# Performance work log

Measured on AMD Instinct MI355X. Metric: run time of the kernel, lower is better.

The kernel has to match this reference:

```python
import jax, jax.numpy as jnp
import numpy as np

B, S, D = 2, 2048, 1024
H, KV, HD = 16, 4, 64
E, TOPK, F = 8, 2, 2048
EPS = 1e-5
THETA = 10000.0


def setup_inputs() -> dict:
    key = jax.random.key(0)
    ks = jax.random.split(key, 12)
    sc = 0.02
    x = jax.random.normal(ks[0], (B, S, D), jnp.float32)
    # real RoPE tables
    inv = 1.0 / (THETA ** (np.arange(0, HD, 2, dtype=np.float32) / HD))
    t = np.arange(S, dtype=np.float32)
    f = np.outer(t, inv)  # [S, HD/2]
    freqs_cos = jnp.asarray(np.cos(f), jnp.float32)
    freqs_sin = jnp.asarray(np.sin(f), jnp.float32)
    return {
        "x": x,
        "freqs_cos": freqs_cos,
        "freqs_sin": freqs_sin,
        "attn_norm_w": jnp.ones((D,), jnp.float32),
        "ffn_norm_w": jnp.ones((D,), jnp.float32),
        "wq": jax.random.normal(ks[1], (D, H * HD), jnp.float32) * sc,
        "wk": jax.random.normal(ks[2], (D, KV * HD), jnp.float32) * sc,
        "wv": jax.random.normal(ks[3], (D, KV * HD), jnp.float32) * sc,
        "wo": jax.random.normal(ks[4], (H * HD, D), jnp.float32) * sc,
        "gate_w": jax.random.normal(ks[5], (D, E), jnp.float32) * sc,
        "w1": jax.random.normal(ks[6], (E, D, F), jnp.float32) * sc,
        "w2": jax.random.normal(ks[7], (E, F, D), jnp.float32) * sc,
        "w3": jax.random.normal(ks[8], (E, D, F), jnp.float32) * sc,
    }


def rmsnorm(x, w):
    return x * jax.lax.rsqrt(jnp.mean(x * x, axis=-1, keepdims=True) + EPS) * w


def apply_rope(xq, cos, sin):
    # xq: [B,S,h,HD]; cos/sin: [S, HD/2]
    xr, xi = xq[..., 0::2], xq[..., 1::2]
    c = cos[None, :, None, :]
    s = sin[None, :, None, :]
    out = jnp.stack([xr * c - xi * s, xr * s + xi * c], axis=-1)
    return out.reshape(xq.shape)


def attention(xn, freqs_cos, freqs_sin, wq, wk, wv, wo):
    q = (xn @ wq).reshape(B, S, H, HD)
    k = (xn @ wk).reshape(B, S, KV, HD)
    v = (xn @ wv).reshape(B, S, KV, HD)
    q = apply_rope(q, freqs_cos, freqs_sin)
    k = apply_rope(k, freqs_cos, freqs_sin)
    n_rep = H // KV
    k = jnp.repeat(k, n_rep, axis=2)  # [B,S,H,HD]
    v = jnp.repeat(v, n_rep, axis=2)
    scores = jnp.einsum("bqhd,bkhd->bhqk", q, k) / jnp.sqrt(jnp.float32(HD))
    causal = jnp.tril(jnp.ones((S, S), bool))
    scores = jnp.where(causal[None, None], scores, jnp.finfo(scores.dtype).min)
    probs = jax.nn.softmax(scores, axis=-1)
    out = jnp.einsum("bhqk,bkhd->bqhd", probs, v).reshape(B, S, H * HD)
    return out @ wo


def sparse_moe(hn, gate_w, w1, w2, w3):
    xf = hn.reshape(-1, D)  # [T, D]
    probs = jax.nn.softmax(xf @ gate_w, axis=-1)  # [T, E]
    topv, topi = jax.lax.top_k(probs, TOPK)
    topv = topv / jnp.sum(topv, axis=-1, keepdims=True)
    # dense [T, E] routing weights (0 for non-selected experts)
    wdense = jnp.sum(jax.nn.one_hot(topi, E, dtype=xf.dtype) * topv[..., None], axis=1)
    h1 = jax.nn.silu(jnp.einsum("td,edf->etf", xf, w1))
    h3 = jnp.einsum("td,edf->etf", xf, w3)
    y = jnp.einsum("etf,efd->etd", h1 * h3, w2)
    out = jnp.einsum("te,etd->td", wdense, y)
    return out.reshape(B, S, D)


def reference(x, freqs_cos, freqs_sin, attn_norm_w, ffn_norm_w,
              wq, wk, wv, wo, gate_w, w1, w2, w3):
    h = x + attention(rmsnorm(x, attn_norm_w), freqs_cos, freqs_sin, wq, wk, wv, wo)
    out = h + sparse_moe(rmsnorm(h, ffn_norm_w), gate_w, w1, w2, w3)
    return out
```

## Files before the change

kernel.cpp:

```cpp
#include <hip/hip_runtime.h>
#include <stdint.h>

typedef unsigned short u16;
typedef unsigned int u32;
typedef __attribute__((ext_vector_type(8))) short short8;
typedef __attribute__((ext_vector_type(8))) u16 us8;
typedef __attribute__((ext_vector_type(4))) u16 us4;
typedef __attribute__((ext_vector_type(4))) float f32x4;

constexpr int NB = 2;
constexpr int SEQ = 2048;
constexpr int DIM = 1024;
constexpr int NH = 16;
constexpr int HD = 64;
constexpr int NE = 8;
constexpr int FF = 2048;
constexpr int TOK = NB * SEQ;
constexpr int NQKV = 1536;
constexpr int NPAIR = TOK * 2;
constexpr float REPS = 1e-5f;

__device__ __forceinline__ u16 f2bf(float x) {
  union { float f; u32 u; } v; v.f = x;
  u32 r = v.u + 0x7fffu + ((v.u >> 16) & 1u);
  return (u16)(r >> 16);
}
__device__ __forceinline__ float bf2f(u16 h) {
  union { u32 u; float f; } v; v.u = ((u32)h) << 16;
  return v.f;
}

__device__ __forceinline__ void gl_lds16(const u16* g, u16* l) {
  __builtin_amdgcn_global_load_lds(
      (const __attribute__((address_space(1))) void*)g,
      (__attribute__((address_space(3))) void*)l, 16, 0, 0);
}

template <bool SPLIT>
__global__ __launch_bounds__(256) void tcvt_k(const float* __restrict__ src,
                                              u16* __restrict__ dhi,
                                              u16* __restrict__ dlo,
                                              int K, int N) {
  int z = blockIdx.z;
  src += (size_t)z * K * N;
  dhi += (size_t)z * K * N;
  if (SPLIT) dlo += (size_t)z * K * N;
  int n0 = blockIdx.x * 64, k0 = blockIdx.y * 64;
  __shared__ float tile[64][65];
  int t = threadIdx.x;
  int kk = t >> 4, nn4 = (t & 15) * 4;
#pragma unroll
  for (int i = 0; i < 4; i++) {
    int k = kk + i * 16;
    const float* p = src + (size_t)(k0 + k) * N + n0 + nn4;
    float4 v = *(const float4*)p;
    tile[nn4 + 0][k] = v.x;
    tile[nn4 + 1][k] = v.y;
    tile[nn4 + 2][k] = v.z;
    tile[nn4 + 3][k] = v.w;
  }
  __syncthreads();
  int nn = t >> 4, k4 = (t & 15) * 4;
#pragma unroll
  for (int i = 0; i < 4; i++) {
    int n = nn + i * 16;
    us4 hi, lo;
#pragma unroll
    for (int j = 0; j < 4; j++) {
      float f = tile[n][k4 + j];
      u16 h = f2bf(f);
      hi[j] = h;
      if (SPLIT) lo[j] = f2bf(f - bf2f(h));
    }
    *(us4*)(dhi + (size_t)(n0 + n) * K + k0 + k4) = hi;
    if (SPLIT) *(us4*)(dlo + (size_t)(n0 + n) * K + k0 + k4) = lo;
  }
}

template <bool SPLIT>
__global__ __launch_bounds__(256) void rmsnorm_k(const float* __restrict__ x,
                                                 const float* __restrict__ w,
                                                 u16* __restrict__ ohi,
                                                 u16* __restrict__ olo) {
  int row = blockIdx.x, t = threadIdx.x;
  float4 v = *(const float4*)(x + (size_t)row * DIM + t * 4);
  float ss = v.x * v.x + v.y * v.y + v.z * v.z + v.w * v.w;
#pragma unroll
  for (int m = 1; m < 64; m <<= 1) ss += __shfl_xor(ss, m);
  __shared__ float red[4];
  if ((t & 63) == 0) red[t >> 6] = ss;
  __syncthreads();
  float rstd = rsqrtf((red[0] + red[1] + red[2] + red[3]) * (1.0f / DIM) + REPS);
  float4 wv = *(const float4*)(w + t * 4);
  float os[4] = {v.x * rstd * wv.x, v.y * rstd * wv.y, v.z * rstd * wv.z,
                 v.w * rstd * wv.w};
  us4 hi, lo;
#pragma unroll
  for (int j = 0; j < 4; j++) {
    u16 h = f2bf(os[j]);
    hi[j] = h;
    if (SPLIT) lo[j] = f2bf(os[j] - bf2f(h));
  }
  *(us4*)(ohi + (size_t)row * DIM + t * 4) = hi;
  if (SPLIT) *(us4*)(olo + (size_t)row * DIM + t * 4) = lo;
}

template <int EPI, bool SPLIT, bool DUAL, bool PERSIST, bool GATHER, int NXL,
          int NT, int BN, int NKS>
__global__ __launch_bounds__(256, 2) void gemm_k(
    const u16* __restrict__ Ah, const u16* __restrict__ Al,
    const u16* __restrict__ Bh, const u16* __restrict__ Bl,
    const u16* __restrict__ Bd, int N, int ldc,
    float* __restrict__ Cf, u16* __restrict__ Cb, float* __restrict__ C2,
    const float* __restrict__ resid, const int* __restrict__ cnt,
    const int* __restrict__ pids, const float* __restrict__ pw,
    const int* __restrict__ plan) {
  constexpr int K = NT * 64;
  constexpr int KT = K * NKS;
  constexpr int WCOL = BN / 2;
  constexpr int FN = BN / 32;

  int tid = threadIdx.x, lane = tid & 63, wid = tid >> 6;
  int wm = wid >> 1, wn = wid & 1;
  int rr = lane & 15, g = lane >> 4;

  __shared__ u16 sAh[128 * 64];
  __shared__ u16 sAl[SPLIT ? 128 * 64 : 16];
  __shared__ u16 sBh[BN * 64];
  __shared__ u16 sBl[SPLIT ? BN * 64 : 16];
  __shared__ u16 sB1[DUAL ? BN * 64 : 16];
  __shared__ int spid[PERSIST ? 128 : 8];
  __shared__ int srow[GATHER ? 128 : 8];

  int pl[9];
  int items;
  if (PERSIST) {
#pragma unroll
    for (int e = 0; e < 9; e++) pl[e] = plan[e];
    items = pl[8] << NXL;
  } else {
    items = 1;
  }

  int it0, itstep;
  if (PERSIST) {
    int nb = gridDim.x;
    it0 = ((nb & 7) == 0) ? ((blockIdx.x & 7) * (nb >> 3) + (blockIdx.x >> 3))
                          : blockIdx.x;
    itstep = nb;
  } else {
    it0 = 0;
    itstep = 1;
  }
  for (int w = it0; w < items; w += itstep) {
    int m0, n0, z, yt, cntz, ks;
    if (PERSIST) {
      int wy = w >> NXL;
      int sub = w & ((1 << NXL) - 1);
      int x = sub / NKS;
      ks = sub % NKS;
      z = 0;
#pragma unroll
      for (int e = 1; e < 8; e++) z += (wy >= pl[e]) ? 1 : 0;
      yt = wy - pl[z];
      m0 = wy * 128;
      n0 = x * BN;
      cntz = cnt[z];
      __syncthreads();
      if (tid < 128) {
        int i = yt * 128 + tid;
        if (i > cntz - 1) i = cntz - 1;
        int p = pids[z * NPAIR + i];
        spid[tid] = p;
        if (GATHER) srow[tid] = p >> 1;
      }
      __syncthreads();
    } else {
      int gx = gridDim.x;
      int nb = gx * gridDim.y;
      int lin = blockIdx.y * gx + blockIdx.x;
      int v = ((nb & 7) == 0) ? ((lin & 7) * (nb >> 3) + (lin >> 3)) : lin;
      m0 = (v / gx) * 128;
      n0 = (v % gx) * BN;
      z = 0;
      yt = 0;
      cntz = 1 << 30;
      ks = 0;
    }

    const u16* Bhz = Bh + (size_t)z * N * KT;
    const u16* Blz = SPLIT ? Bl + (size_t)z * N * KT : nullptr;
    const u16* Bdz = DUAL ? Bd + (size_t)z * N * KT : nullptr;
    int kbase = ks * K;

    const u16 *agh[4], *agl[SPLIT ? 4 : 1];
    int aoff[4];
#pragma unroll
    for (int i = 0; i < 4; i++) {
      int cid = tid + i * 256;
      int r = cid >> 3, c = cid & 7;
      int gr = GATHER ? srow[r] : (m0 + r);
      int sc = c ^ (r & 7);
      agh[i] = Ah + (size_t)gr * KT + kbase + sc * 8;
      if (SPLIT) agl[i] = Al + (size_t)gr * KT + kbase + sc * 8;
      aoff[i] = r * 64 + c * 8;
    }
    const u16 *bgh[FN], *bgl[SPLIT ? FN : 1], *bg1[DUAL ? FN : 1];
    int boff[FN];
#pragma unroll
    for (int i = 0; i < FN; i++) {
      int cid = tid + i * 256;
      int r = cid >> 3, c = cid & 7;
      int sc = c ^ (r & 7);
      size_t gr = (size_t)(n0 + r) * KT + kbase + sc * 8;
      bgh[i] = Bhz + gr;
      if (SPLIT) bgl[i] = Blz + gr;
      if (DUAL) bg1[i] = Bdz + gr;
      boff[i] = r * 64 + c * 8;
    }

    f32x4 zv = {0.f, 0.f, 0.f, 0.f};
    f32x4 acc[4][FN];
    f32x4 acc1[DUAL ? 4 : 1][DUAL ? FN : 1];
#pragma unroll
    for (int a = 0; a < 4; a++)
#pragma unroll
      for (int b = 0; b < FN; b++) {
        acc[a][b] = zv;
        if (DUAL) acc1[a][b] = zv;
      }

    for (int t = 0; t < NT; t++) {
      int k0 = t * 64;
      __syncthreads();
#pragma unroll
      for (int i = 0; i < 4; i++) {
        gl_lds16(agh[i] + k0, sAh + aoff[i]);
        if (SPLIT) gl_lds16(agl[i] + k0, sAl + aoff[i]);
      }
#pragma unroll
      for (int i = 0; i < FN; i++) {
        gl_lds16(bgh[i] + k0, sBh + boff[i]);
        if (SPLIT) gl_lds16(bgl[i] + k0, sBl + boff[i]);
        if (DUAL) gl_lds16(bg1[i] + k0, sB1 + boff[i]);
      }
      __syncthreads();

#pragma unroll
      for (int kc = 0; kc < 2; kc++) {
        short8 a_h[4], a_l[SPLIT ? 4 : 1], b_h[FN], b_l[SPLIT ? FN : 1],
            b1f[DUAL ? FN : 1];
#pragma unroll
        for (int f = 0; f < 4; f++) {
          int ra = wm * 64 + f * 16 + rr;
          int off = ra * 64 + (((kc * 4 + g) ^ (ra & 7)) * 8);
          a_h[f] = *(const short8*)&sAh[off];
          if (SPLIT) a_l[f] = *(const short8*)&sAl[off];
        }
#pragma unroll
        for (int f = 0; f < FN; f++) {
          int rb = wn * WCOL + f * 16 + rr;
          int off = rb * 64 + (((kc * 4 + g) ^ (rb & 7)) * 8);
          b_h[f] = *(const short8*)&sBh[off];
          if (SPLIT) b_l[f] = *(const short8*)&sBl[off];
          if (DUAL) b1f[f] = *(const short8*)&sB1[off];
        }
#pragma unroll
        for (int fm = 0; fm < 4; fm++)
#pragma unroll
          for (int fn = 0; fn < FN; fn++) {
            acc[fm][fn] = __builtin_amdgcn_mfma_f32_16x16x32_bf16(
                a_h[fm], b_h[fn], acc[fm][fn], 0, 0, 0);
            if (SPLIT) {
              acc[fm][fn] = __builtin_amdgcn_mfma_f32_16x16x32_bf16(
                  a_h[fm], b_l[fn], acc[fm][fn], 0, 0, 0);
              acc[fm][fn] = __builtin_amdgcn_mfma_f32_16x16x32_bf16(
                  a_l[fm], b_h[fn], acc[fm][fn], 0, 0, 0);
            }
            if (DUAL)
              acc1[fm][fn] = __builtin_amdgcn_mfma_f32_16x16x32_bf16(
                  a_h[fm], b1f[fn], acc1[fm][fn], 0, 0, 0);
          }
      }
    }

#pragma unroll
    for (int fm = 0; fm < 4; fm++)
#pragma unroll
      for (int fn = 0; fn < FN; fn++)
#pragma unroll
        for (int rg = 0; rg < 4; rg++) {
          int rl = wm * 64 + fm * 16 + g * 4 + rg;
          int col = n0 + wn * WCOL + fn * 16 + rr;
          float v = acc[fm][fn][rg];
          if (EPI == 0) {
            Cf[(size_t)(m0 + rl) * ldc + col] = v;
          } else if (EPI == 1) {
            size_t idx = (size_t)(m0 + rl) * ldc + col;
            float r2 = v + resid[idx];
            Cf[idx] = r2;
            C2[idx] = r2;
          } else if (EPI == 2) {
            float gg = v / (1.0f + __expf(-v));
            float o = gg * acc1[fm][fn][rg];
            Cb[(size_t)(m0 + rl) * ldc + col] = f2bf(o);
          } else {
            int i = yt * 128 + rl;
            if (i < cntz) {
              int p = spid[rl];
              atomicAdd(&Cf[(size_t)(p >> 1) * ldc + col], pw[p] * v);
            }
          }
        }
  }
}

__global__ __launch_bounds__(256) void rope_k(float* __restrict__ qkv,
                                              const float* __restrict__ fc,
                                              const float* __restrict__ fs) {
  int idx = blockIdx.x * 256 + threadIdx.x;
  int i = idx & 31;
  int hh = (idx >> 5) % 20;
  int t = idx / 640;
  if (t >= TOK) return;
  int s = t & (SEQ - 1);
  int base = (hh < 16) ? (hh * 64) : (1024 + (hh - 16) * 64);
  float c = fc[s * 32 + i], sn = fs[s * 32 + i];
  float* p = qkv + (size_t)t * NQKV + base + 2 * i;
  float xr = p[0], xi = p[1];
  p[0] = xr * c - xi * sn;
  p[1] = xr * sn + xi * c;
}

__global__ __launch_bounds__(256) void cvtkv_k(const float* __restrict__ qkv,
                                               u16* __restrict__ Kh,
                                               u16* __restrict__ Kl,
                                               u16* __restrict__ Vh,
                                               u16* __restrict__ Vl) {
  int kvt = blockIdx.x;
  int kvh = blockIdx.y;
  int b = blockIdx.z;
  int t = threadIdx.x;
  __shared__ float vt[64][65];
  size_t tile = ((size_t)((b * 4 + kvh) * 32 + kvt)) * 4096;
  int r = t >> 2, c4 = t & 3;
  {
    const float* kp = qkv + ((size_t)(b * SEQ + kvt * 64 + r)) * NQKV + 1024 +
                      kvh * 64 + c4 * 16;
    float ff[16];
#pragma unroll
    for (int q = 0; q < 4; q++) {
      float4 f = *(const float4*)(kp + q * 4);
      ff[q * 4 + 0] = f.x; ff[q * 4 + 1] = f.y;
      ff[q * 4 + 2] = f.z; ff[q * 4 + 3] = f.w;
    }
#pragma unroll
    for (int half = 0; half < 2; half++) {
      int c = c4 * 2 + half;
      us8 hi, lo;
#pragma unroll
      for (int j = 0; j < 8; j++) {
        float f = ff[half * 8 + j];
        u16 h = f2bf(f);
        hi[j] = h;
        lo[j] = f2bf(f - bf2f(h));
      }
      int off = r * 64 + ((c ^ (r & 7)) * 8);
      *(us8*)(Kh + tile + off) = hi;
      *(us8*)(Kl + tile + off) = lo;
    }
  }
  {
    const float* vp = qkv + ((size_t)(b * SEQ + kvt * 64 + r)) * NQKV + 1280 +
                      kvh * 64 + c4 * 16;
#pragma unroll
    for (int q = 0; q < 4; q++) {
      float4 f = *(const float4*)(vp + q * 4);
      vt[r][c4 * 16 + q * 4 + 0] = f.x;
      vt[r][c4 * 16 + q * 4 + 1] = f.y;
      vt[r][c4 * 16 + q * 4 + 2] = f.z;
      vt[r][c4 * 16 + q * 4 + 3] = f.w;
    }
  }
  __syncthreads();
  {
    int d = t >> 2, g4 = t & 3;
    float ff[16];
#pragma unroll
    for (int j = 0; j < 16; j++) ff[j] = vt[g4 * 16 + j][d];
#pragma unroll
    for (int half = 0; half < 2; half++) {
      int c = g4 * 2 + half;
      us8 hi, lo;
#pragma unroll
      for (int j = 0; j < 8; j++) {
        float f = ff[half * 8 + j];
        u16 h = f2bf(f);
        hi[j] = h;
        lo[j] = f2bf(f - bf2f(h));
      }
      int off = d * 64 + ((c ^ (d & 7)) * 8);
      *(us8*)(Vh + tile + off) = hi;
      *(us8*)(Vl + tile + off) = lo;
    }
  }
}

__global__ __launch_bounds__(256, 2) void flash_k(
    const float* __restrict__ qkv, const u16* __restrict__ Kg,
    const u16* __restrict__ Klg, const u16* __restrict__ Vg,
    const u16* __restrict__ Vlg, u16* __restrict__ ah, u16* __restrict__ al) {
  int pi = blockIdx.x;
  int h = blockIdx.y;
  int b = blockIdx.z;
  int qt[2] = {31 - pi, pi};
  int kvh = h >> 2;
  int tid = threadIdx.x, lane = tid & 63, wid = tid >> 6;
  int rr = lane & 15, g = lane >> 4;

  __shared__ u16 sKh[4096], sKl[4096], sVh[4096], sVl[4096];
  __shared__ u32 sP[4][16 * 67];

  f32x4 zv = {0.f, 0.f, 0.f, 0.f};
  short8 aqh[2][2], aql[2][2];
#pragma unroll
  for (int u = 0; u < 2; u++) {
    int qrow = qt[u] * 64 + wid * 16 + rr;
    const float* qp =
        qkv + ((size_t)(b * SEQ + qrow)) * NQKV + h * 64 + g * 8;
#pragma unroll
    for (int kc = 0; kc < 2; kc++) {
      float4 f0 = *(const float4*)(qp + kc * 32);
      float4 f1 = *(const float4*)(qp + kc * 32 + 4);
      float ff[8] = {f0.x, f0.y, f0.z, f0.w, f1.x, f1.y, f1.z, f1.w};
#pragma unroll
      for (int j = 0; j < 8; j++) {
        u16 hi = f2bf(ff[j]);
        aqh[u][kc][j] = (short)hi;
        aql[u][kc][j] = (short)f2bf(ff[j] - bf2f(hi));
      }
    }
  }

  f32x4 o[2][4];
  float m_r[2][4], l_r[2][4];
#pragma unroll
  for (int u = 0; u < 2; u++)
#pragma unroll
    for (int i = 0; i < 4; i++) {
      o[u][i] = zv;
      m_r[u][i] = -3.0e38f;
      l_r[u][i] = 0.f;
    }

  size_t tb = ((size_t)(b * 4 + kvh) * 32) * 4096;
  int so = tid * 16;
  us8 rKh[2], rKl[2], rVh[2], rVl[2];
  {
    size_t go = tb + so;
    rKh[0] = *(const us8*)(Kg + go);  rKh[1] = *(const us8*)(Kg + go + 8);
    rKl[0] = *(const us8*)(Klg + go); rKl[1] = *(const us8*)(Klg + go + 8);
    rVh[0] = *(const us8*)(Vg + go);  rVh[1] = *(const us8*)(Vg + go + 8);
    rVl[0] = *(const us8*)(Vlg + go); rVl[1] = *(const us8*)(Vlg + go + 8);
  }

  int nt = qt[0];
  for (int kvt = 0; kvt <= nt; kvt++) {
    __syncthreads();
    *(us8*)&sKh[so] = rKh[0]; *(us8*)&sKh[so + 8] = rKh[1];
    *(us8*)&sKl[so] = rKl[0]; *(us8*)&sKl[so + 8] = rKl[1];
    *(us8*)&sVh[so] = rVh[0]; *(us8*)&sVh[so + 8] = rVh[1];
    *(us8*)&sVl[so] = rVl[0]; *(us8*)&sVl[so + 8] = rVl[1];
    if (kvt < nt) {
      size_t go = tb + (size_t)(kvt + 1) * 4096 + so;
      rKh[0] = *(const us8*)(Kg + go);  rKh[1] = *(const us8*)(Kg + go + 8);
      rKl[0] = *(const us8*)(Klg + go); rKl[1] = *(const us8*)(Klg + go + 8);
      rVh[0] = *(const us8*)(Vg + go);  rVh[1] = *(const us8*)(Vg + go + 8);
      rVl[0] = *(const us8*)(Vlg + go); rVl[1] = *(const us8*)(Vlg + go + 8);
    }
    __syncthreads();

#pragma unroll
    for (int u = 0; u < 2; u++) {
      if (!(u == 1 && kvt > qt[1])) {
        float pv[4][4];
        __builtin_amdgcn_s_setprio(1);
#pragma unroll
        for (int c16 = 0; c16 < 4; c16++) {
          int rk = c16 * 16 + rr;
          f32x4 sacc = zv;
#pragma unroll
          for (int kc = 0; kc < 2; kc++) {
            int sw = rk * 64 + (((kc * 4 + g) ^ (rk & 7)) * 8);
            short8 bh = *(const short8*)&sKh[sw];
            short8 bl = *(const short8*)&sKl[sw];
            sacc = __builtin_amdgcn_mfma_f32_16x16x32_bf16(aqh[u][kc], bh,
                                                           sacc, 0, 0, 0);
            sacc = __builtin_amdgcn_mfma_f32_16x16x32_bf16(aqh[u][kc], bl,
                                                           sacc, 0, 0, 0);
            sacc = __builtin_amdgcn_mfma_f32_16x16x32_bf16(aql[u][kc], bh,
                                                           sacc, 0, 0, 0);
          }
          bool diag = (kvt == qt[u]);
#pragma unroll
          for (int rg = 0; rg < 4; rg++) {
            float val = sacc[rg] * 0.125f;
            if (diag) {
              int kv_l = c16 * 16 + rr;
              int q_l = wid * 16 + g * 4 + rg;
              if (kv_l > q_l) val = -3.0e38f;
            }
            pv[c16][rg] = val;
          }
        }
        __builtin_amdgcn_s_setprio(0);
        float pm[4];
#pragma unroll
        for (int rg = 0; rg < 4; rg++)
          pm[rg] = fmaxf(fmaxf(pv[0][rg], pv[1][rg]),
                         fmaxf(pv[2][rg], pv[3][rg]));
#pragma unroll
        for (int m = 1; m < 16; m <<= 1)
#pragma unroll
          for (int rg = 0; rg < 4; rg++)
            pm[rg] = fmaxf(pm[rg], __shfl_xor(pm[rg], m));
        bool dok = true;
#pragma unroll
        for (int rg = 0; rg < 4; rg++)
          dok = dok && (pm[rg] - m_r[u][rg] <= 8.0f);
        if (!__all(dok)) {
          float scl[4];
#pragma unroll
          for (int rg = 0; rg < 4; rg++) {
            float mn = fmaxf(m_r[u][rg], pm[rg]);
            scl[rg] = __expf(m_r[u][rg] - mn);
            m_r[u][rg] = mn;
          }
#pragma unroll
          for (int rg = 0; rg < 4; rg++) l_r[u][rg] *= scl[rg];
#pragma unroll
          for (int d16 = 0; d16 < 4; d16++)
#pragma unroll
            for (int rg = 0; rg < 4; rg++) o[u][d16][rg] *= scl[rg];
        }
#pragma unroll
        for (int c16 = 0; c16 < 4; c16++)
#pragma unroll
          for (int rg = 0; rg < 4; rg++)
            pv[c16][rg] = __expf(pv[c16][rg] - m_r[u][rg]);
        float rsum[4];
#pragma unroll
        for (int rg = 0; rg < 4; rg++)
          rsum[rg] = pv[0][rg] + pv[1][rg] + pv[2][rg] + pv[3][rg];
#pragma unroll
        for (int m = 1; m < 16; m <<= 1)
#pragma unroll
          for (int rg = 0; rg < 4; rg++) rsum[rg] += __shfl_xor(rsum[rg], m);
#pragma unroll
        for (int rg = 0; rg < 4; rg++) l_r[u][rg] += rsum[rg];

#pragma unroll
        for (int c16 = 0; c16 < 4; c16++)
#pragma unroll
          for (int rg = 0; rg < 4; rg++) {
            int ql = g * 4 + rg;
            int kvl = c16 * 16 + rr;
            u16 hi = f2bf(pv[c16][rg]);
            u16 lo = f2bf(pv[c16][rg] - bf2f(hi));
            sP[wid][ql * 67 + kvl] = ((u32)lo << 16) | (u32)hi;
          }
        short8 pah[2], pal[2];
#pragma unroll
        for (int kc = 0; kc < 2; kc++) {
          const u32* pp = &sP[wid][rr * 67 + kc * 32 + g * 8];
#pragma unroll
          for (int j = 0; j < 8; j++) {
            u32 w = pp[j];
            pah[kc][j] = (short)(w & 0xffffu);
            pal[kc][j] = (short)(w >> 16);
          }
        }
        __builtin_amdgcn_s_setprio(1);
#pragma unroll
        for (int d16 = 0; d16 < 4; d16++) {
          int rv = d16 * 16 + rr;
#pragma unroll
          for (int kc = 0; kc < 2; kc++) {
            int sw = rv * 64 + (((kc * 4 + g) ^ (rv & 7)) * 8);
            short8 vh = *(const short8*)&sVh[sw];
            short8 vl = *(const short8*)&sVl[sw];
            o[u][d16] = __builtin_amdgcn_mfma_f32_16x16x32_bf16(
                pah[kc], vh, o[u][d16], 0, 0, 0);
            o[u][d16] = __builtin_amdgcn_mfma_f32_16x16x32_bf16(
                pah[kc], vl, o[u][d16], 0, 0, 0);
            o[u][d16] = __builtin_amdgcn_mfma_f32_16x16x32_bf16(
                pal[kc], vh, o[u][d16], 0, 0, 0);
          }
        }
        __builtin_amdgcn_s_setprio(0);
      }
    }
  }

#pragma unroll
  for (int u = 0; u < 2; u++)
#pragma unroll
    for (int rg = 0; rg < 4; rg++) {
      float inv = 1.0f / l_r[u][rg];
      int qr = qt[u] * 64 + wid * 16 + g * 4 + rg;
      size_t obase = (size_t)(b * SEQ + qr) * 1024 + h * 64;
#pragma unroll
      for (int d16 = 0; d16 < 4; d16++) {
        float v = o[u][d16][rg] * inv;
        u16 hi = f2bf(v);
        ah[obase + d16 * 16 + rr] = hi;
        al[obase + d16 * 16 + rr] = f2bf(v - bf2f(hi));
      }
    }
}

__global__ __launch_bounds__(256) void route_k(const float* __restrict__ h,
                                               const float* __restrict__ wffn,
                                               const float* __restrict__ gw,
                                               int* __restrict__ cnt,
                                               int* __restrict__ pids,
                                               float* __restrict__ pw) {
  int t = blockIdx.x, tid = threadIdx.x;
  float4 v = *(const float4*)(h + (size_t)t * DIM + tid * 4);
  float ss = v.x * v.x + v.y * v.y + v.z * v.z + v.w * v.w;
#pragma unroll
  for (int m = 1; m < 64; m <<= 1) ss += __shfl_xor(ss, m);
  __shared__ float red[4];
  if ((tid & 63) == 0) red[tid >> 6] = ss;
  __syncthreads();
  float rstd = rsqrtf((red[0] + red[1] + red[2] + red[3]) * (1.0f / DIM) + REPS);
  float4 wv = *(const float4*)(wffn + tid * 4);
  float xn[4] = {v.x * rstd * wv.x, v.y * rstd * wv.y, v.z * rstd * wv.z,
                 v.w * rstd * wv.w};
  float pl[8] = {0, 0, 0, 0, 0, 0, 0, 0};
#pragma unroll
  for (int j = 0; j < 4; j++) {
    const float* gp = gw + (size_t)(tid * 4 + j) * 8;
    float4 g0 = *(const float4*)gp;
    float4 g1 = *(const float4*)(gp + 4);
    pl[0] += xn[j] * g0.x; pl[1] += xn[j] * g0.y;
    pl[2] += xn[j] * g0.z; pl[3] += xn[j] * g0.w;
    pl[4] += xn[j] * g1.x; pl[5] += xn[j] * g1.y;
    pl[6] += xn[j] * g1.z; pl[7] += xn[j] * g1.w;
  }
#pragma unroll
  for (int e = 0; e < 8; e++)
#pragma unroll
    for (int m = 1; m < 64; m <<= 1) pl[e] += __shfl_xor(pl[e], m);
  __shared__ float lred[4][8];
  if ((tid & 63) == 0)
#pragma unroll
    for (int e = 0; e < 8; e++) lred[tid >> 6][e] = pl[e];
  __syncthreads();
  if (tid == 0) {
    float lg[8];
#pragma unroll
    for (int e = 0; e < 8; e++)
      lg[e] = lred[0][e] + lred[1][e] + lred[2][e] + lred[3][e];
    int e1 = 0;
    float l1 = lg[0];
#pragma unroll
    for (int e = 1; e < 8; e++)
      if (lg[e] > l1) { l1 = lg[e]; e1 = e; }
    int e2 = -1;
    float l2 = -3.0e38f;
#pragma unroll
    for (int e = 0; e < 8; e++)
      if (e != e1 && lg[e] > l2) { l2 = lg[e]; e2 = e; }
    float w1 = 1.0f / (1.0f + expf(l2 - l1));
    float w2 = 1.0f / (1.0f + expf(l1 - l2));
    int p0 = atomicAdd(&cnt[e1], 1);
    pids[e1 * NPAIR + p0] = t * 2;
    pw[t * 2] = w1;
    int p1 = atomicAdd(&cnt[e2], 1);
    pids[e2 * NPAIR + p1] = t * 2 + 1;
    pw[t * 2 + 1] = w2;
  }
}

__global__ void zero_k(int* cnt) {
  if (threadIdx.x < 8) cnt[threadIdx.x] = 0;
}

__global__ void plan_k(const int* __restrict__ cnt, int* __restrict__ plan) {
  if (threadIdx.x == 0) {
    int acc = 0;
    for (int e = 0; e < 8; e++) {
      plan[e] = acc;
      acc += (cnt[e] + 127) >> 7;
    }
    plan[8] = acc;
  }
}

extern "C" void kernel_launch(void* const* d_in, const int* in_sizes, int n_in,
                              void* d_out, int out_size, void* d_ws,
                              size_t ws_size, hipStream_t stream) {
  (void)in_sizes; (void)n_in; (void)out_size; (void)ws_size;
  const float* x = (const float*)d_in[0];
  const float* fc = (const float*)d_in[1];
  const float* fs = (const float*)d_in[2];
  const float* anw = (const float*)d_in[3];
  const float* fnw = (const float*)d_in[4];
  const float* wq = (const float*)d_in[5];
  const float* wk = (const float*)d_in[6];
  const float* wv = (const float*)d_in[7];
  const float* wo = (const float*)d_in[8];
  const float* gw = (const float*)d_in[9];
  const float* w1 = (const float*)d_in[10];
  const float* w2 = (const float*)d_in[11];
  const float* w3 = (const float*)d_in[12];
  float* outf = (float*)d_out;

  char* ws = (char*)d_ws;
  size_t off = 0;
  auto alloc = [&](size_t bytes) {
    void* p = ws + off;
    off += (bytes + 255) & ~(size_t)255;
    return p;
  };
  u16* xnh = (u16*)alloc((size_t)TOK * DIM * 2);
  u16* xnl = (u16*)alloc((size_t)TOK * DIM * 2);
  float* qkvf = (float*)alloc((size_t)TOK * NQKV * 4);
  u16* h13 = xnh;
  u16* wqkvT_h = (u16*)alloc((size_t)NQKV * DIM * 2);
  u16* wqkvT_l = (u16*)alloc((size_t)NQKV * DIM * 2);
  u16* woT_h = (u16*)alloc((size_t)DIM * DIM * 2);
  u16* woT_l = (u16*)alloc((size_t)DIM * DIM * 2);
  u16* w1T = (u16*)alloc((size_t)NE * FF * DIM * 2);
  u16* w3T = (u16*)alloc((size_t)NE * FF * DIM * 2);
  u16* w2T = (u16*)alloc((size_t)NE * DIM * FF * 2);
  u16* attnh = (u16*)alloc((size_t)TOK * DIM * 2);
  u16* attnl = (u16*)alloc((size_t)TOK * DIM * 2);
  float* hbuf = (float*)alloc((size_t)TOK * DIM * 4);
  u16* hn = (u16*)alloc((size_t)TOK * DIM * 2);
  int* cnt = (int*)alloc(64);
  int* plan = (int*)alloc(64);
  int* pids = (int*)alloc((size_t)NE * NPAIR * 4);
  float* pwbuf = (float*)alloc((size_t)NPAIR * 4);
  u16* Ksw_h = (u16*)alloc((size_t)NB * 4 * SEQ * 64 * 2);
  u16* Ksw_l = (u16*)alloc((size_t)NB * 4 * SEQ * 64 * 2);
  u16* Vsw_h = (u16*)alloc((size_t)NB * 4 * SEQ * 64 * 2);
  u16* Vsw_l = (u16*)alloc((size_t)NB * 4 * SEQ * 64 * 2);

  dim3 blk(256);
  hipLaunchKernelGGL((tcvt_k<true>), dim3(16, 16, 1), blk, 0, stream, wq,
                     wqkvT_h, wqkvT_l, 1024, 1024);
  hipLaunchKernelGGL((tcvt_k<true>), dim3(4, 16, 1), blk, 0, stream, wk,
                     wqkvT_h + 1024 * 1024, wqkvT_l + 1024 * 1024, 1024, 256);
  hipLaunchKernelGGL((tcvt_k<true>), dim3(4, 16, 1), blk, 0, stream, wv,
                     wqkvT_h + 1280 * 1024, wqkvT_l + 1280 * 1024, 1024, 256);
  hipLaunchKernelGGL((tcvt_k<true>), dim3(16, 16, 1), blk, 0, stream, wo, woT_h,
                     woT_l, 1024, 1024);
  hipLaunchKernelGGL((tcvt_k<false>), dim3(32, 16, 8), blk, 0, stream, w1, w1T,
                     (u16*)nullptr, 1024, 2048);
  hipLaunchKernelGGL((tcvt_k<false>), dim3(32, 16, 8), blk, 0, stream, w3, w3T,
                     (u16*)nullptr, 1024, 2048);
  hipLaunchKernelGGL((tcvt_k<false>), dim3(16, 32, 8), blk, 0, stream, w2, w2T,
                     (u16*)nullptr, 2048, 1024);
  hipLaunchKernelGGL((rmsnorm_k<true>), dim3(TOK), blk, 0, stream, x, anw, xnh,
                     xnl);
  hipLaunchKernelGGL((gemm_k<0, true, false, false, false, 0, 16, 64, 1>),
                     dim3(NQKV / 64, TOK / 128, 1), blk, 0, stream, xnh, xnl,
                     wqkvT_h, wqkvT_l, (const u16*)nullptr, NQKV, NQKV, qkvf,
                     (u16*)nullptr, (float*)nullptr, (const float*)nullptr,
                     (const int*)nullptr, (const int*)nullptr,
                     (const float*)nullptr, (const int*)nullptr);
  hipLaunchKernelGGL(rope_k, dim3((TOK * 20 * 32) / 256), blk, 0, stream, qkvf,
                     fc, fs);
  hipLaunchKernelGGL(cvtkv_k, dim3(SEQ / 64, 4, NB), blk, 0, stream, qkvf,
                     Ksw_h, Ksw_l, Vsw_h, Vsw_l);
  hipLaunchKernelGGL(flash_k, dim3(16, NH, NB), blk, 0, stream, qkvf, Ksw_h,
                     Ksw_l, Vsw_h, Vsw_l, attnh, attnl);
  hipLaunchKernelGGL((gemm_k<1, true, false, false, false, 0, 16, 64, 1>),
                     dim3(DIM / 64, TOK / 128, 1), blk, 0, stream, attnh, attnl,
                     woT_h, woT_l, (const u16*)nullptr, DIM, DIM, hbuf,
                     (u16*)nullptr, outf, x, (const int*)nullptr,
                     (const int*)nullptr, (const float*)nullptr,
                     (const int*)nullptr);
  hipLaunchKernelGGL((rmsnorm_k<false>), dim3(TOK), blk, 0, stream, hbuf, fnw,
                     hn, (u16*)nullptr);
  hipLaunchKernelGGL(zero_k, dim3(1), dim3(64), 0, stream, cnt);
  hipLaunchKernelGGL(route_k, dim3(TOK), blk, 0, stream, hbuf, fnw, gw, cnt,
                     pids, pwbuf);
  hipLaunchKernelGGL(plan_k, dim3(1), dim3(64), 0, stream, cnt, plan);
  hipLaunchKernelGGL((gemm_k<2, false, true, true, true, 4, 16, 128, 1>),
                     dim3(1024), blk, 0, stream, hn, (const u16*)nullptr, w1T,
                     (const u16*)nullptr, w3T, FF, FF, (float*)nullptr, h13,
                     (float*)nullptr, (const float*)nullptr, cnt, pids, pwbuf,
                     plan);
  hipLaunchKernelGGL((gemm_k<3, false, false, true, false, 4, 16, 128, 2>),
                     dim3(1152), blk, 0, stream, h13, (const u16*)nullptr, w2T,
                     (const u16*)nullptr, (const u16*)nullptr, DIM, DIM, outf,
                     (u16*)nullptr, (float*)nullptr, (const float*)nullptr, cnt,
                     pids, pwbuf, plan);
}
```

Before: 556.7 us.

## Split flash attention KV loop across two blocks and add merge kernel

The causal flash-attention grid doubles. Each block now handles every other KV tile (even or odd) and writes unnormalized partial outputs plus its row max and row sum to scratch. A new merge kernel rescales and combines the two partials, normalizes, and writes the hi/lo bf16 attention output. This targets the low block count of the attention kernel, which leaves CUs idle. The cost is 32 MB of fp32 partial traffic, one extra launch, and reusing the hbuf/hn region as o_part scratch.

```diff
diff --git a/kernel.cpp b/kernel.cpp
--- a/kernel.cpp
+++ b/kernel.cpp
@@ -409,10 +409,13 @@
 __global__ __launch_bounds__(256, 2) void flash_k(
     const float* __restrict__ qkv, const u16* __restrict__ Kg,
     const u16* __restrict__ Klg, const u16* __restrict__ Vg,
-    const u16* __restrict__ Vlg, u16* __restrict__ ah, u16* __restrict__ al) {
+    const u16* __restrict__ Vlg, float* __restrict__ o_part,
+    float* __restrict__ m_part, float* __restrict__ l_part) {
   int pi = blockIdx.x;
   int h = blockIdx.y;
-  int b = blockIdx.z;
+  int bh = blockIdx.z;
+  int b = bh & 1;
+  int half = bh >> 1;
   int qt[2] = {31 - pi, pi};
   int kvh = h >> 2;
   int tid = threadIdx.x, lane = tid & 63, wid = tid >> 6;
@@ -455,24 +458,24 @@
 
   size_t tb = ((size_t)(b * 4 + kvh) * 32) * 4096;
   int so = tid * 16;
+  int nt = qt[0];
   us8 rKh[2], rKl[2], rVh[2], rVl[2];
-  {
-    size_t go = tb + so;
+  if (half <= nt) {
+    size_t go = tb + (size_t)half * 4096 + so;
     rKh[0] = *(const us8*)(Kg + go);  rKh[1] = *(const us8*)(Kg + go + 8);
     rKl[0] = *(const us8*)(Klg + go); rKl[1] = *(const us8*)(Klg + go + 8);
     rVh[0] = *(const us8*)(Vg + go);  rVh[1] = *(const us8*)(Vg + go + 8);
     rVl[0] = *(const us8*)(Vlg + go); rVl[1] = *(const us8*)(Vlg + go + 8);
   }
 
-  int nt = qt[0];
-  for (int kvt = 0; kvt <= nt; kvt++) {
+  for (int kvt = half; kvt <= nt; kvt += 2) {
     __syncthreads();
     *(us8*)&sKh[so] = rKh[0]; *(us8*)&sKh[so + 8] = rKh[1];
     *(us8*)&sKl[so] = rKl[0]; *(us8*)&sKl[so + 8] = rKl[1];
     *(us8*)&sVh[so] = rVh[0]; *(us8*)&sVh[so + 8] = rVh[1];
     *(us8*)&sVl[so] = rVl[0]; *(us8*)&sVl[so + 8] = rVl[1];
-    if (kvt < nt) {
-      size_t go = tb + (size_t)(kvt + 1) * 4096 + so;
+    if (kvt + 2 <= nt) {
+      size_t go = tb + (size_t)(kvt + 2) * 4096 + so;
       rKh[0] = *(const us8*)(Kg + go);  rKh[1] = *(const us8*)(Kg + go + 8);
       rKl[0] = *(const us8*)(Klg + go); rKl[1] = *(const us8*)(Klg + go + 8);
       rVh[0] = *(const us8*)(Vg + go);  rVh[1] = *(const us8*)(Vg + go + 8);
@@ -492,13 +495,13 @@
 #pragma unroll
           for (int kc = 0; kc < 2; kc++) {
             int sw = rk * 64 + (((kc * 4 + g) ^ (rk & 7)) * 8);
-            short8 bh = *(const short8*)&sKh[sw];
+            short8 bh2 = *(const short8*)&sKh[sw];
             short8 bl = *(const short8*)&sKl[sw];
-            sacc = __builtin_amdgcn_mfma_f32_16x16x32_bf16(aqh[u][kc], bh,
+            sacc = __builtin_amdgcn_mfma_f32_16x16x32_bf16(aqh[u][kc], bh2,
                                                            sacc, 0, 0, 0);
             sacc = __builtin_amdgcn_mfma_f32_16x16x32_bf16(aqh[u][kc], bl,
                                                            sacc, 0, 0, 0);
-            sacc = __builtin_amdgcn_mfma_f32_16x16x32_bf16(aql[u][kc], bh,
+            sacc = __builtin_amdgcn_mfma_f32_16x16x32_bf16(aql[u][kc], bh2,
                                                            sacc, 0, 0, 0);
           }
           bool diag = (kvt == qt[u]);
@@ -602,21 +605,56 @@
     }
   }
 
+  int H2 = half * NB + b;
 #pragma unroll
   for (int u = 0; u < 2; u++)
 #pragma unroll
     for (int rg = 0; rg < 4; rg++) {
-      float inv = 1.0f / l_r[u][rg];
       int qr = qt[u] * 64 + wid * 16 + g * 4 + rg;
-      size_t obase = (size_t)(b * SEQ + qr) * 1024 + h * 64;
-#pragma unroll
-      for (int d16 = 0; d16 < 4; d16++) {
-        float v = o[u][d16][rg] * inv;
-        u16 hi = f2bf(v);
-        ah[obase + d16 * 16 + rr] = hi;
-        al[obase + d16 * 16 + rr] = f2bf(v - bf2f(hi));
-      }
-    }
+      size_t mlidx = ((size_t)H2 * SEQ + qr) * NH + h;
+      if (rr == 0) {
+        m_part[mlidx] = m_r[u][rg];
+        l_part[mlidx] = l_r[u][rg];
+      }
+      size_t obase = mlidx * 64;
+#pragma unroll
+      for (int d16 = 0; d16 < 4; d16++)
+        o_part[obase + d16 * 16 + rr] = o[u][d16][rg];
+    }
+}
+
+__global__ __launch_bounds__(256) void merge_k(const float* __restrict__ o_part,
+                                               const float* __restrict__ m_part,
+                                               const float* __restrict__ l_part,
+                                               u16* __restrict__ ah,
+                                               u16* __restrict__ al) {
+  int idx = blockIdx.x * 256 + threadIdx.x;
+  int d4 = idx & 15;
+  int h = (idx >> 4) & 15;
+  int t = idx >> 8;
+  int b = t >> 11;
+  int qr = t & (SEQ - 1);
+  size_t i0 = ((size_t)(0 * NB + b) * SEQ + qr) * NH + h;
+  size_t i1 = ((size_t)(1 * NB + b) * SEQ + qr) * NH + h;
+  float m1 = m_part[i0], l1 = l_part[i0];
+  float m2 = m_part[i1], l2 = l_part[i1];
+  float mm = fmaxf(m1, m2);
+  float w1 = __expf(m1 - mm), w2 = __expf(m2 - mm);
+  float inv = 1.0f / (l1 * w1 + l2 * w2);
+  float4 o1 = *(const float4*)(o_part + i0 * 64 + d4 * 4);
+  float4 o2 = *(const float4*)(o_part + i1 * 64 + d4 * 4);
+  float out[4] = {(o1.x * w1 + o2.x * w2) * inv, (o1.y * w1 + o2.y * w2) * inv,
+                  (o1.z * w1 + o2.z * w2) * inv, (o1.w * w1 + o2.w * w2) * inv};
+  us4 hi, lo;
+#pragma unroll
+  for (int j = 0; j < 4; j++) {
+    u16 hh = f2bf(out[j]);
+    hi[j] = hh;
+    lo[j] = f2bf(out[j] - bf2f(hh));
+  }
+  size_t ad = (size_t)t * DIM + h * 64 + d4 * 4;
+  *(us4*)(ah + ad) = hi;
+  *(us4*)(al + ad) = lo;
 }
 
 __global__ __launch_bounds__(256) void route_k(const float* __restrict__ h,
@@ -737,8 +775,6 @@
   u16* w2T = (u16*)alloc((size_t)NE * DIM * FF * 2);
   u16* attnh = (u16*)alloc((size_t)TOK * DIM * 2);
   u16* attnl = (u16*)alloc((size_t)TOK * DIM * 2);
-  float* hbuf = (float*)alloc((size_t)TOK * DIM * 4);
-  u16* hn = (u16*)alloc((size_t)TOK * DIM * 2);
   int* cnt = (int*)alloc(64);
   int* plan = (int*)alloc(64);
   int* pids = (int*)alloc((size_t)NE * NPAIR * 4);
@@ -747,6 +783,12 @@
   u16* Ksw_l = (u16*)alloc((size_t)NB * 4 * SEQ * 64 * 2);
   u16* Vsw_h = (u16*)alloc((size_t)NB * 4 * SEQ * 64 * 2);
   u16* Vsw_l = (u16*)alloc((size_t)NB * 4 * SEQ * 64 * 2);
+  float* m_part = (float*)alloc((size_t)2 * TOK * NH * 4);
+  float* l_part = (float*)alloc((size_t)2 * TOK * NH * 4);
+  float* hbuf = (float*)alloc((size_t)TOK * DIM * 4);
+  u16* hn = (u16*)alloc((size_t)TOK * DIM * 2);
+  (void)alloc((size_t)8 * 1024 * 1024);
+  float* o_part = hbuf;
 
   dim3 blk(256);
   hipLaunchKernelGGL((tcvt_k<true>), dim3(16, 16, 1), blk, 0, stream, wq,
@@ -775,8 +817,10 @@
                      fc, fs);
   hipLaunchKernelGGL(cvtkv_k, dim3(SEQ / 64, 4, NB), blk, 0, stream, qkvf,
                      Ksw_h, Ksw_l, Vsw_h, Vsw_l);
-  hipLaunchKernelGGL(flash_k, dim3(16, NH, NB), blk, 0, stream, qkvf, Ksw_h,
-                     Ksw_l, Vsw_h, Vsw_l, attnh, attnl);
+  hipLaunchKernelGGL(flash_k, dim3(16, NH, NB * 2), blk, 0, stream, qkvf,
+                     Ksw_h, Ksw_l, Vsw_h, Vsw_l, o_part, m_part, l_part);
+  hipLaunchKernelGGL(merge_k, dim3(TOK * NH * 16 / 256), blk, 0, stream,
+                     o_part, m_part, l_part, attnh, attnl);
   hipLaunchKernelGGL((gemm_k<1, true, false, false, false, 0, 16, 64, 1>),
                      dim3(DIM / 64, TOK / 128, 1), blk, 0, stream, attnh, attnl,
                      woT_h, woT_l, (const u16*)nullptr, DIM, DIM, hbuf,
```

Result: slower. 569.4 us (+2.3%).
